# Kernel optimization log

Measured on AMD Instinct MI355X. Metric: run time of the kernel, lower is better.

Reference implementation:

```python
import jax, jax.numpy as jnp
import numpy as np

N = 20000   # nodes
E = 400000  # edges per hop
IN_C = 256
HID = 128
HEADS = 2
OUT_C = 256
RELU_SLOPE = 0.2  # GATConv LeakyReLU negative slope
EPS = 1e-16


def _segment_mean(vals, idx, num_segments):
    s = jax.ops.segment_sum(vals, idx, num_segments=num_segments)
    cnt = jax.ops.segment_sum(jnp.ones((vals.shape[0], 1), vals.dtype), idx,
                              num_segments=num_segments)
    return s / (cnt + EPS)


def _gat(x, src, dst, Wg, a_src, a_dst, bg):
    # x: [N, IN_C] -> h: [N, HEADS, HID]
    h = (x @ Wg).reshape(N, HEADS, HID)
    alpha_s = jnp.sum(h * a_src, axis=-1)  # [N, HEADS]
    alpha_d = jnp.sum(h * a_dst, axis=-1)  # [N, HEADS]
    logits = jax.nn.leaky_relu(alpha_s[src] + alpha_d[dst], RELU_SLOPE)  # [E, HEADS]
    # softmax over incoming edges per destination node
    m = jax.ops.segment_max(logits, dst, num_segments=N)  # [N, HEADS]
    m = jnp.where(jnp.isfinite(m), m, 0.0)
    ex = jnp.exp(logits - m[dst])
    denom = jax.ops.segment_sum(ex, dst, num_segments=N)  # [N, HEADS]
    alpha = ex / (denom[dst] + EPS)  # [E, HEADS]
    msg = h[src] * alpha[..., None]  # [E, HEADS, HID]
    out = jax.ops.segment_sum(msg, dst, num_segments=N)  # [N, HEADS, HID]
    return out.reshape(N, HEADS * HID) + bg


def setup_inputs() -> dict:
    key = jax.random.key(0)
    ks = jax.random.split(key, 16)

    def xav(k, shape):
        fan_in, fan_out = shape[0], shape[-1]
        lim = np.sqrt(6.0 / (fan_in + fan_out)).astype(np.float32)
        return jax.random.uniform(k, shape, jnp.float32, -lim, lim)

    inp = {
        "x": jax.random.normal(ks[0], (N, IN_C), jnp.float32),
        "edge_index_1hop": jax.random.randint(ks[1], (2, E), 0, N),
        "edge_time_1hop": jax.random.uniform(ks[2], (E,), jnp.float32),
        "edge_index_2hop": jax.random.randint(ks[3], (2, E), 0, N),
        "edge_time_2hop": jax.random.uniform(ks[4], (E,), jnp.float32),
        "rel_embeddings": jax.random.normal(ks[5], (N, HID), jnp.float32),
        # GATConv params
        "Wg": xav(ks[6], (IN_C, HEADS * HID)),
        "a_src": jax.random.normal(ks[7], (HEADS, HID), jnp.float32) * 0.1,
        "a_dst": jax.random.normal(ks[8], (HEADS, HID), jnp.float32) * 0.1,
        "bg": jnp.zeros((HEADS * HID,), jnp.float32),
        # linear_transform
        "W_lin": xav(ks[9], (HEADS * HID, OUT_C)),
        "b_lin": jnp.zeros((OUT_C,), jnp.float32),
        # time_gate: in = 2*(OUT_C+1)
        "W_tg": xav(ks[10], (2 * (OUT_C + 1), 1)),
        "b_tg": jnp.zeros((1,), jnp.float32),
        # semantic_gate: in = (OUT_C+1) + HID + 1
        "W_sg": xav(ks[11], (OUT_C + 1 + HID + 1, 1)),
        "b_sg": jnp.zeros((1,), jnp.float32),
    }
    return inp


def reference(x, edge_index_1hop, edge_time_1hop, edge_index_2hop,
              edge_time_2hop, rel_embeddings, Wg, a_src, a_dst, bg,
              W_lin, b_lin, W_tg, b_tg, W_sg, b_sg):
    src1, dst1 = edge_index_1hop[0], edge_index_1hop[1]
    src2, dst2 = edge_index_2hop[0], edge_index_2hop[1]

    # ---- 1-hop aggregation ----
    x_1hop = _gat(x, src1, dst1, Wg, a_src, a_dst, bg) @ W_lin + b_lin  # [N, OUT_C]
    time_e1 = edge_time_1hop[:, None]  # [E, 1]
    node_time = _segment_mean(time_e1, dst1, N)  # [N, 1]
    x_1hop_t = jnp.concatenate([x_1hop, node_time], axis=-1)  # [N, OUT_C+1]

    # ---- semantic gate (per 1-hop edge -> per node) ----
    combined = jnp.concatenate(
        [x_1hop_t[src1], rel_embeddings[dst1], time_e1], axis=-1)  # [E, OUT_C+1+HID+1]
    sem_w_edge = jax.nn.sigmoid(combined @ W_sg + b_sg)  # [E, 1]
    sem_w_node = _segment_mean(sem_w_edge, dst1, N)  # [N, 1]

    # ---- 2-hop aggregation, semantically weighted ----
    x_2hop = _gat(x, src2, dst2, Wg, a_src, a_dst, bg) @ W_lin + b_lin  # [N, OUT_C]
    x_2hop = x_2hop * sem_w_node
    x_2hop_t = jnp.concatenate([x_2hop, node_time], axis=-1)  # [N, OUT_C+1]

    # ---- time-gated fusion ----
    gate_in = jnp.concatenate([x_1hop_t, x_2hop_t], axis=-1)  # [N, 2*(OUT_C+1)]
    g = jax.nn.sigmoid(gate_in @ W_tg + b_tg)  # [N, 1]
    return g * x_2hop_t + (1.0 - g) * x_1hop_t
```

## Files before the change

### kernel.cpp

```cpp
#include <hip/hip_runtime.h>
#include <math.h>

constexpr float EPSF = 1e-16f;
#define MAXDEG 64
#define BINCH 4096
#define NBUCK 64

typedef __attribute__((ext_vector_type(8))) short bfrag;
typedef __attribute__((ext_vector_type(4))) float ffrag;
typedef __attribute__((ext_vector_type(8))) unsigned short ushortv8;

__device__ __forceinline__ float leaky(float v){ return v >= 0.f ? v : 0.2f*v; }

__device__ __forceinline__ ushort f2bf(float f){
  union { float f; unsigned u; } v; v.f = f;
  unsigned r = (v.u + 0x7FFFu + ((v.u >> 16) & 1u)) >> 16;
  return (ushort)r;
}
__device__ __forceinline__ float bf2f(ushort u){
  union { unsigned u; float f; } v; v.u = ((unsigned)u) << 16;
  return v.f;
}

__device__ __forceinline__ float wred_max(float v){
  #pragma unroll
  for (int d = 32; d; d >>= 1) v = fmaxf(v, __shfl_xor(v, d));
  return v;
}
__device__ __forceinline__ float wred_sum(float v){
  #pragma unroll
  for (int d = 32; d; d >>= 1) v += __shfl_xor(v, d);
  return v;
}


__global__ __launch_bounds__(256) void k_prep(const float* __restrict__ Wg, const float* __restrict__ Wlin,
    const float* __restrict__ rel, const float* __restrict__ Wsg,
    ushort* __restrict__ Wgt, ushort* __restrict__ Wlt, float* __restrict__ p2, int N){
  __shared__ float tile[32][33];
  int b = blockIdx.x, t = threadIdx.x;
  if (b < 128){
    const float* W = (b < 64) ? Wg : Wlin;
    ushort* Wt = (b < 64) ? Wgt : Wlt;
    int bb = b & 63;
    int bx = (bb & 7)*32, by = (bb >> 3)*32;
    int tx = t & 31, ty = t >> 5;
    for (int r = ty; r < 32; r += 8) tile[r][tx] = W[(size_t)(by+r)*256 + bx+tx];
    __syncthreads();
    for (int r = ty; r < 32; r += 8) Wt[(size_t)(bx+r)*256 + by+tx] = f2bf(tile[tx][r]);
  } else {
    int node = (b-128)*4 + (t>>6);
    if (node >= N) return;
    int lane = t & 63;
    const float* rr = rel + (size_t)node*128;
    float q = rr[lane]*Wsg[257+lane] + rr[64+lane]*Wsg[321+lane];
    q = wred_sum(q);
    if (lane == 0) p2[node] = q;
  }
}


__global__ __launch_bounds__(256) void k_work1(const float* __restrict__ x, const ushort* __restrict__ Wgt,
    const float* __restrict__ a_src, const float* __restrict__ a_dst,
    ushort* __restrict__ hb, float* __restrict__ as_, float* __restrict__ ad_,
    const int* __restrict__ ei1, const float* __restrict__ et1, const int* __restrict__ ei2,
    int* __restrict__ gcur, int2* __restrict__ bkt1, int2* __restrict__ bkt2,
    int cap1, int cap2, int N, int E1, int E2, int GB1, int B1, int NB){
  __shared__ int hist[NBUCK];
  __shared__ int loff[NBUCK+1];
  __shared__ int cur[NBUCK];
  __shared__ int gbase_s[NBUCK];
  __shared__ int2 stage[BINCH];
  int bid = blockIdx.x, t = threadIdx.x;
  if (bid >= GB1){
    int hop = (bid >= GB1 + B1);
    int cb  = hop ? (bid - GB1 - B1) : (bid - GB1);
    const int* src_arr = hop ? ei2 : ei1;
    const int* dst_arr = hop ? (ei2 + E2) : (ei1 + E1);
    int Eh = hop ? E2 : E1;
    int c0 = cb * BINCH;
    int M = Eh - c0; if (M > BINCH) M = BINCH;
    if (t < NBUCK) hist[t] = 0;
    __syncthreads();
    #pragma unroll
    for (int k = 0; k < BINCH/256; k++){
      int i = k*256 + t;
      if (i < M) atomicAdd(&hist[dst_arr[c0 + i] / NB], 1);
    }
    __syncthreads();
    if (t < NBUCK){
      int v = hist[t];
      int xx = v;
      #pragma unroll
      for (int d = 1; d < NBUCK; d <<= 1){
        int y = __shfl_up(xx, d);
        if (t >= d) xx += y;
      }
      loff[t+1] = xx;
      if (t == 0) loff[0] = 0;
      cur[t] = xx - v;
      gbase_s[t] = atomicAdd(&gcur[hop*NBUCK + t], v);
    }
    __syncthreads();
    #pragma unroll
    for (int k = 0; k < BINCH/256; k++){
      int i = k*256 + t;
      if (i < M){
        int s = src_arr[c0 + i];
        int d = dst_arr[c0 + i];
        int b = d / NB;
        int ld = d - b*NB;
        int pos = atomicAdd(&cur[b], 1);
        float tv = hop ? 0.f : et1[c0 + i];
        stage[pos] = make_int2(s | (ld << 15), __float_as_int(tv));
      }
    }
    __syncthreads();
    int2* bkt = hop ? bkt2 : bkt1;
    int cap = hop ? cap2 : cap1;
    for (int s = t; s < M; s += 256){
      int lo = 0, hi = NBUCK;
      while (hi - lo > 1){ int mid = (lo + hi) >> 1; if (loff[mid] <= s) lo = mid; else hi = mid; }
      int gpos = gbase_s[lo] + (s - loff[lo]);
      if (gpos < cap) bkt[(size_t)lo*cap + gpos] = stage[s];
    }
    return;
  }
  int head = bid & 1;
  int bx = bid >> 1;
  int wid = t >> 6, lane = t & 63;
  int wr = wid >> 1, wc = wid & 1;
  int row0 = bx*128 + wr*64;
  int col0 = head*128 + wc*64;
  int l15 = lane & 15, lk = lane >> 4;
  ffrag acc[4][4];
  #pragma unroll
  for (int i = 0; i < 4; i++)
    #pragma unroll
    for (int j = 0; j < 4; j++){ ffrag z; z[0]=0.f; z[1]=0.f; z[2]=0.f; z[3]=0.f; acc[i][j] = z; }
  for (int kk = 0; kk < 256; kk += 32){
    bfrag a[4], b[4];
    #pragma unroll
    for (int i = 0; i < 4; i++){
      int r = row0 + i*16 + l15; if (r > N-1) r = N-1;
      float4 u0 = *(const float4*)(x + (size_t)r*256 + kk + lk*8);
      float4 u1 = *(const float4*)(x + (size_t)r*256 + kk + lk*8 + 4);
      bfrag tv;
      tv[0]=(short)f2bf(u0.x); tv[1]=(short)f2bf(u0.y); tv[2]=(short)f2bf(u0.z); tv[3]=(short)f2bf(u0.w);
      tv[4]=(short)f2bf(u1.x); tv[5]=(short)f2bf(u1.y); tv[6]=(short)f2bf(u1.z); tv[7]=(short)f2bf(u1.w);
      a[i] = tv;
      int c = col0 + i*16 + l15;
      b[i] = *(const bfrag*)(Wgt + (size_t)c*256 + kk + lk*8);
    }
    #pragma unroll
    for (int i = 0; i < 4; i++)
      #pragma unroll
      for (int j = 0; j < 4; j++)
        acc[i][j] = __builtin_amdgcn_mfma_f32_16x16x32_bf16(a[i], b[j], acc[i][j], 0, 0, 0);
  }
  float asv[4], adv[4];
  #pragma unroll
  for (int j = 0; j < 4; j++){
    int cc = wc*64 + j*16 + l15;
    asv[j] = a_src[head*128 + cc];
    adv[j] = a_dst[head*128 + cc];
  }
  #pragma unroll
  for (int i = 0; i < 4; i++){
    float ps[4] = {0.f,0.f,0.f,0.f}, pd[4] = {0.f,0.f,0.f,0.f};
    #pragma unroll
    for (int j = 0; j < 4; j++){
      int c = col0 + j*16 + l15;
      #pragma unroll
      for (int q = 0; q < 4; q++){
        int r = row0 + i*16 + lk*4 + q;
        float v = acc[i][j][q];
        if (r < N) hb[(size_t)r*256 + c] = f2bf(v);
        ps[q] = fmaf(v, asv[j], ps[q]);
        pd[q] = fmaf(v, adv[j], pd[q]);
      }
    }
    #pragma unroll
    for (int q = 0; q < 4; q++){
      #pragma unroll
      for (int d = 1; d < 16; d <<= 1){
        ps[q] += __shfl_xor(ps[q], d);
        pd[q] += __shfl_xor(pd[q], d);
      }
      int r = row0 + i*16 + lk*4 + q;
      if (l15 == 0 && r < N){
        atomicAdd(&as_[r*2 + head], ps[q]);
        atomicAdd(&ad_[r*2 + head], pd[q]);
      }
    }
  }
}


__global__ __launch_bounds__(256) void k_place(const int* __restrict__ gcur,
    const int2* __restrict__ bkt1, const int2* __restrict__ bkt2, int cap1, int cap2,
    int* __restrict__ ssrc1, int* __restrict__ ssrc2, float* __restrict__ stime1,
    int* __restrict__ cntg, float* __restrict__ ntime, float* __restrict__ p1,
    const float* __restrict__ Wsg, int N, int NB){
  __shared__ int   cnt_l[512];
  __shared__ float ts_l[512];
  int b = blockIdx.x & 63, hop = blockIdx.x >> 6;
  int t = threadIdx.x;
  int nbase = b * NB;
  int ncnt = N - nbase; if (ncnt > NB) ncnt = NB; if (ncnt < 0) ncnt = 0;
  for (int i = t; i < NB; i += 256){ cnt_l[i] = 0; ts_l[i] = 0.f; }
  __syncthreads();
  const int2* bkt = hop ? bkt2 : bkt1;
  int cap = hop ? cap2 : cap1;
  int len = gcur[hop*NBUCK + b]; if (len > cap) len = cap;
  int* ssrc = hop ? ssrc2 : ssrc1;
  for (int i = t; i < len; i += 256){
    int2 en = bkt[(size_t)b*cap + i];
    int src = en.x & 0x7FFF;
    int ld  = en.x >> 15;
    int slot = atomicAdd(&cnt_l[ld], 1);
    if (slot < MAXDEG){
      size_t o = (size_t)(nbase + ld)*MAXDEG + slot;
      ssrc[o] = src;
      if (hop == 0) stime1[o] = __int_as_float(en.y);
    }
    if (hop == 0) atomicAdd(&ts_l[ld], __int_as_float(en.y));
  }
  __syncthreads();
  float w256 = Wsg[256];
  for (int ld = t; ld < ncnt; ld += 256){
    int node = nbase + ld;
    int c = cnt_l[ld];
    cntg[hop*N + node] = c;
    if (hop == 0){
      float nt = ts_l[ld] / ((float)c + EPSF);
      ntime[node] = nt;
      p1[node] = nt * w256;
    }
  }
}


__global__ __launch_bounds__(256) void k_node(const int* __restrict__ cntg,
    const int* __restrict__ ssrc1, const int* __restrict__ ssrc2,
    const float* __restrict__ as_, const float* __restrict__ ad_,
    const ushort* __restrict__ h, const float* __restrict__ bg,
    ushort* __restrict__ gatb, int N, int gN4){
  __shared__ int   s_src[4][MAXDEG];
  __shared__ float2 s_w[4][MAXDEG];
  int wid = threadIdx.x >> 6, lane = threadIdx.x & 63;
  int hop = blockIdx.x >= gN4;
  int node = (blockIdx.x - (hop ? gN4 : 0))*4 + wid;
  bool active = node < N;
  const int* ssrc = hop ? ssrc2 : ssrc1;
  int deg = 0; float ad0 = 0.f, ad1 = 0.f;
  if (active){
    int degt = cntg[hop*N + node];
    deg = degt > MAXDEG ? MAXDEG : degt;
    ad0 = ad_[node*2]; ad1 = ad_[node*2+1];
  }
  size_t o0 = (size_t)node * MAXDEG;
  int msrc = 0;
  float l0 = -INFINITY, l1 = -INFINITY;
  if (lane < deg){
    msrc = ssrc[o0 + lane];
    float2 a = ((const float2*)as_)[msrc];
    l0 = leaky(a.x + ad0); l1 = leaky(a.y + ad1);
  }
  float m0 = wred_max(l0), m1 = wred_max(l1);
  float x0 = 0.f, x1 = 0.f;
  if (lane < deg){ x0 = __expf(l0 - m0); x1 = __expf(l1 - m1); }
  float e0 = wred_sum(x0), e1 = wred_sum(x1);
  float rd0 = 1.f/(e0 + EPSF), rd1 = 1.f/(e1 + EPSF);
  s_src[wid][lane] = msrc;
  s_w[wid][lane] = make_float2(x0*rd0, x1*rd1);
  if (!active) return;
  int eh = lane >> 5, cl = lane & 31, ch0 = cl << 3, head = cl >> 4;
  float acc[8] = {0.f,0.f,0.f,0.f,0.f,0.f,0.f,0.f};
  int i = 0;
  for (; i + 4 <= deg; i += 4){
    int eA = i + eh, eB = i + 2 + eh;
    int sA = s_src[wid][eA], sB = s_src[wid][eB];
    float2 wA2 = s_w[wid][eA], wB2 = s_w[wid][eB];
    float wA = head ? wA2.y : wA2.x;
    float wB = head ? wB2.y : wB2.x;
    ushortv8 uA = *(const ushortv8*)(h + (size_t)sA*256 + ch0);
    ushortv8 uB = *(const ushortv8*)(h + (size_t)sB*256 + ch0);
    #pragma unroll
    for (int k = 0; k < 8; k++) acc[k] = fmaf(wA, bf2f(uA[k]), acc[k]);
    #pragma unroll
    for (int k = 0; k < 8; k++) acc[k] = fmaf(wB, bf2f(uB[k]), acc[k]);
  }
  for (; i < deg; i += 2){
    int e = i + eh;
    bool v = e < deg;
    int s = v ? s_src[wid][e] : 0;
    float w = 0.f;
    if (v){ float2 w2 = s_w[wid][e]; w = head ? w2.y : w2.x; }
    ushortv8 u = *(const ushortv8*)(h + (size_t)s*256 + ch0);
    #pragma unroll
    for (int k = 0; k < 8; k++) acc[k] = fmaf(w, bf2f(u[k]), acc[k]);
  }
  #pragma unroll
  for (int k = 0; k < 8; k++) acc[k] += __shfl_xor(acc[k], 32);
  if (eh == 0){
    float4 b0 = *(const float4*)(bg + ch0);
    float4 b1 = *(const float4*)(bg + ch0 + 4);
    ushortv8 o;
    o[0] = f2bf(acc[0] + b0.x); o[1] = f2bf(acc[1] + b0.y);
    o[2] = f2bf(acc[2] + b0.z); o[3] = f2bf(acc[3] + b0.w);
    o[4] = f2bf(acc[4] + b1.x); o[5] = f2bf(acc[5] + b1.y);
    o[6] = f2bf(acc[6] + b1.z); o[7] = f2bf(acc[7] + b1.w);
    *(ushortv8*)(gatb + (size_t)(hop ? N + node : node)*256 + ch0) = o;
  }
}


__global__ __launch_bounds__(256) void k_gemm2(const ushort* __restrict__ A, const ushort* __restrict__ Bt,
    const float* __restrict__ bias, const float* __restrict__ Wsg,
    float* __restrict__ Cf, float* __restrict__ p1, int M, int N){
  int wid = threadIdx.x >> 6, lane = threadIdx.x & 63;
  int wr = wid >> 1, wc = wid & 1;
  int row0 = blockIdx.x*128 + wr*64;
  int col0 = blockIdx.y*128 + wc*64;
  int l15 = lane & 15, lk = lane >> 4;
  ffrag acc[4][4];
  #pragma unroll
  for (int i = 0; i < 4; i++)
    #pragma unroll
    for (int j = 0; j < 4; j++){ ffrag z; z[0]=0.f; z[1]=0.f; z[2]=0.f; z[3]=0.f; acc[i][j] = z; }
  for (int kk = 0; kk < 256; kk += 32){
    bfrag a[4], b[4];
    #pragma unroll
    for (int i = 0; i < 4; i++){
      int r = row0 + i*16 + l15; if (r > M-1) r = M-1;
      a[i] = *(const bfrag*)(A + (size_t)r*256 + kk + lk*8);
      int c = col0 + i*16 + l15;
      b[i] = *(const bfrag*)(Bt + (size_t)c*256 + kk + lk*8);
    }
    #pragma unroll
    for (int i = 0; i < 4; i++)
      #pragma unroll
      for (int j = 0; j < 4; j++)
        acc[i][j] = __builtin_amdgcn_mfma_f32_16x16x32_bf16(a[i], b[j], acc[i][j], 0, 0, 0);
  }
  float wsv[4]; float bv[4];
  #pragma unroll
  for (int j = 0; j < 4; j++){
    int c = col0 + j*16 + l15;
    wsv[j] = Wsg[c];
    bv[j] = bias[c];
  }
  #pragma unroll
  for (int i = 0; i < 4; i++){
    float ps[4] = {0.f,0.f,0.f,0.f};
    #pragma unroll
    for (int j = 0; j < 4; j++){
      int c = col0 + j*16 + l15;
      #pragma unroll
      for (int q = 0; q < 4; q++){
        int r = row0 + i*16 + lk*4 + q;
        float v = acc[i][j][q] + bv[j];
        if (r < M) Cf[(size_t)r*256 + c] = v;
        ps[q] = fmaf(v, wsv[j], ps[q]);
      }
    }
    #pragma unroll
    for (int q = 0; q < 4; q++){
      #pragma unroll
      for (int d = 1; d < 16; d <<= 1) ps[q] += __shfl_xor(ps[q], d);
      int r = row0 + i*16 + lk*4 + q;
      if (l15 == 0 && r < N) atomicAdd(&p1[r], ps[q]);
    }
  }
}


__global__ __launch_bounds__(256) void k_final(const float* __restrict__ x1, const float* __restrict__ x2r,
    const int* __restrict__ cntg, const int* __restrict__ ssrc1, const float* __restrict__ stime1,
    const float* __restrict__ p1, const float* __restrict__ p2,
    const float* __restrict__ Wsg, const float* __restrict__ bsg,
    const float* __restrict__ ntime, const float* __restrict__ Wtg, const float* __restrict__ btg,
    float* __restrict__ out, int N){
  int node = blockIdx.x*4 + (threadIdx.x>>6);
  if (node >= N) return;
  int lane = threadIdx.x & 63;
  int degt = cntg[node];
  int deg = degt > MAXDEG ? MAXDEG : degt;
  float acc = 0.f;
  if (lane < deg){
    size_t o = (size_t)node*MAXDEG + lane;
    float z = p1[ssrc1[o]] + p2[node] + bsg[0] + stime1[o]*Wsg[385];
    acc = 1.f / (1.f + __expf(-z));
  }
  acc = wred_sum(acc);
  float sm = acc / ((float)degt + EPSF);
  float nt = ntime[node];
  int c0 = lane << 2;
  float4 a4 = *(const float4*)(x1  + (size_t)node*256 + c0);
  float4 r4 = *(const float4*)(x2r + (size_t)node*256 + c0);
  float4 b4; b4.x = r4.x*sm; b4.y = r4.y*sm; b4.z = r4.z*sm; b4.w = r4.w*sm;
  float4 w1 = *(const float4*)(Wtg + c0);
  float4 w2 = *(const float4*)(Wtg + 257 + c0);
  float s = a4.x*w1.x + a4.y*w1.y + a4.z*w1.z + a4.w*w1.w
          + b4.x*w2.x + b4.y*w2.y + b4.z*w2.z + b4.w*w2.w;
  if (lane == 0) s += nt*Wtg[256] + nt*Wtg[513] + btg[0];
  s = wred_sum(s);
  float g = 1.f / (1.f + __expf(-s));
  float* orow = out + (size_t)node*257;
  orow[c0+0] = g*b4.x + (1.f - g)*a4.x;
  orow[c0+1] = g*b4.y + (1.f - g)*a4.y;
  orow[c0+2] = g*b4.z + (1.f - g)*a4.z;
  orow[c0+3] = g*b4.w + (1.f - g)*a4.w;
  if (lane == 0) orow[256] = nt;
}


extern "C" void kernel_launch(void* const* d_in, const int* in_sizes, int n_in,
                              void* d_out, int out_size, void* d_ws, size_t ws_size,
                              hipStream_t stream){
  const float* x    = (const float*)d_in[0];
  const int*   ei1  = (const int*)d_in[1];
  const float* et1  = (const float*)d_in[2];
  const int*   ei2  = (const int*)d_in[3];
  const float* rel  = (const float*)d_in[5];
  const float* Wg   = (const float*)d_in[6];
  const float* asrc = (const float*)d_in[7];
  const float* adst = (const float*)d_in[8];
  const float* bg   = (const float*)d_in[9];
  const float* Wlin = (const float*)d_in[10];
  const float* blin = (const float*)d_in[11];
  const float* Wtg  = (const float*)d_in[12];
  const float* btg  = (const float*)d_in[13];
  const float* Wsg  = (const float*)d_in[14];
  const float* bsg  = (const float*)d_in[15];
  float* out = (float*)d_out;

  const int N  = in_sizes[0] / 256;
  const int E1 = in_sizes[1] / 2;
  const int E2 = in_sizes[3] / 2;
  const int NB = (N + NBUCK - 1) / NBUCK;
  const int cap1 = E1/NBUCK + 2048;
  const int cap2 = E2/NBUCK + 2048;

  char* base = (char*)d_ws;
  size_t off = 0;
  auto alloc = [&](size_t bytes)->char*{
    char* p = base + off;
    off += (bytes + 255) & ~(size_t)255;
    return p;
  };
  int*    gcur  = (int*)alloc((size_t)2*NBUCK*4);
  float*  as_   = (float*)alloc((size_t)2*N*4);
  float*  ad_   = (float*)alloc((size_t)2*N*4);
  size_t zero_bytes = off;
  ushort* Wgt   = (ushort*)alloc((size_t)256*256*2);
  ushort* Wlt   = (ushort*)alloc((size_t)256*256*2);
  ushort* hb    = (ushort*)alloc((size_t)N*256*2);
  ushort* gatb  = (ushort*)alloc((size_t)2*N*256*2);
  float*  x12   = (float*)alloc((size_t)2*N*256*4);
  float*  ntime = (float*)alloc((size_t)N*4);
  float*  p1    = (float*)alloc((size_t)N*4);
  float*  p2    = (float*)alloc((size_t)N*4);
  int*    cntg  = (int*)alloc((size_t)2*N*4);
  int*    ssrc1 = (int*)alloc((size_t)N*MAXDEG*4);
  int*    ssrc2 = (int*)alloc((size_t)N*MAXDEG*4);
  float*  stime1= (float*)alloc((size_t)N*MAXDEG*4);
  int2*   bkt1  = (int2*)alloc((size_t)NBUCK*cap1*8);
  int2*   bkt2  = (int2*)alloc((size_t)NBUCK*cap2*8);

  dim3 blk(256);
  int gN4 = (N + 3) / 4;
  int GB1 = ((N + 127) / 128) * 2;
  int B1  = (E1 + BINCH - 1) / BINCH;
  int B2  = (E2 + BINCH - 1) / BINCH;
  dim3 ggemm2((2*N + 127) / 128, 2);

  hipMemsetAsync(d_ws, 0, zero_bytes, stream);
  k_prep<<<128 + gN4, blk, 0, stream>>>(Wg, Wlin, rel, Wsg, Wgt, Wlt, p2, N);
  k_work1<<<GB1 + B1 + B2, blk, 0, stream>>>(x, Wgt, asrc, adst, hb, as_, ad_,
                                             ei1, et1, ei2, gcur, bkt1, bkt2,
                                             cap1, cap2, N, E1, E2, GB1, B1, NB);
  k_place<<<128, blk, 0, stream>>>(gcur, bkt1, bkt2, cap1, cap2, ssrc1, ssrc2, stime1,
                                   cntg, ntime, p1, Wsg, N, NB);
  k_node<<<2*gN4, blk, 0, stream>>>(cntg, ssrc1, ssrc2, as_, ad_, hb, bg, gatb, N, gN4);
  k_gemm2<<<ggemm2, blk, 0, stream>>>(gatb, Wlt, blin, Wsg, x12, p1, 2*N, N);
  k_final<<<gN4, blk, 0, stream>>>(x12, x12 + (size_t)N*256, cntg, ssrc1, stime1,
                                   p1, p2, Wsg, bsg, ntime, Wtg, btg, out, N);
}
```

Before: 158.1 us.

## Store GEMM2 output in bf16, fold workspace zeroing into prep, unroll gather

The second GEMM now writes its output to an intermediate buffer as bf16 instead of fp32, and the final kernel reads bf16 and converts, halving that buffer's traffic. The hipMemsetAsync is replaced by extra blocks in k_prep that zero the workspace, removing a separate memset launch. The node aggregation loop gains an 8-edge unrolled body that issues four gathers per lane at once to raise memory-level parallelism. The cost is reduced precision of the intermediate x1/x2 values and higher register pressure.

After: 149.4 us. -5.5%, faster.

```diff
diff --git a/kernel.cpp b/kernel.cpp
--- a/kernel.cpp
+++ b/kernel.cpp
@@ -36,20 +36,25 @@
 
 __global__ __launch_bounds__(256) void k_prep(const float* __restrict__ Wg, const float* __restrict__ Wlin,
     const float* __restrict__ rel, const float* __restrict__ Wsg,
-    ushort* __restrict__ Wgt, ushort* __restrict__ Wlt, float* __restrict__ p2, int N){
+    ushort* __restrict__ Wgt, ushort* __restrict__ Wlt, float* __restrict__ p2,
+    float4* __restrict__ zbase, int znum4, int ZB, int N){
   __shared__ float tile[32][33];
   int b = blockIdx.x, t = threadIdx.x;
-  if (b < 128){
-    const float* W = (b < 64) ? Wg : Wlin;
-    ushort* Wt = (b < 64) ? Wgt : Wlt;
-    int bb = b & 63;
+  if (b < ZB){
+    int idx = b*256 + t;
+    if (idx < znum4) zbase[idx] = make_float4(0.f,0.f,0.f,0.f);
+  } else if (b < ZB + 128){
+    int bb = b - ZB;
+    const float* W = (bb < 64) ? Wg : Wlin;
+    ushort* Wt = (bb < 64) ? Wgt : Wlt;
+    bb &= 63;
     int bx = (bb & 7)*32, by = (bb >> 3)*32;
     int tx = t & 31, ty = t >> 5;
     for (int r = ty; r < 32; r += 8) tile[r][tx] = W[(size_t)(by+r)*256 + bx+tx];
     __syncthreads();
     for (int r = ty; r < 32; r += 8) Wt[(size_t)(bx+r)*256 + by+tx] = f2bf(tile[tx][r]);
   } else {
-    int node = (b-128)*4 + (t>>6);
+    int node = (b-ZB-128)*4 + (t>>6);
     if (node >= N) return;
     int lane = t & 63;
     const float* rr = rel + (size_t)node*128;
@@ -278,6 +283,29 @@
   int eh = lane >> 5, cl = lane & 31, ch0 = cl << 3, head = cl >> 4;
   float acc[8] = {0.f,0.f,0.f,0.f,0.f,0.f,0.f,0.f};
   int i = 0;
+  for (; i + 8 <= deg; i += 8){
+    int eA = i + eh, eB = i + 2 + eh, eC = i + 4 + eh, eD = i + 6 + eh;
+    int sA = s_src[wid][eA], sB = s_src[wid][eB];
+    int sC = s_src[wid][eC], sD = s_src[wid][eD];
+    float2 wA2 = s_w[wid][eA], wB2 = s_w[wid][eB];
+    float2 wC2 = s_w[wid][eC], wD2 = s_w[wid][eD];
+    float wA = head ? wA2.y : wA2.x;
+    float wB = head ? wB2.y : wB2.x;
+    float wC = head ? wC2.y : wC2.x;
+    float wD = head ? wD2.y : wD2.x;
+    ushortv8 uA = *(const ushortv8*)(h + (size_t)sA*256 + ch0);
+    ushortv8 uB = *(const ushortv8*)(h + (size_t)sB*256 + ch0);
+    ushortv8 uC = *(const ushortv8*)(h + (size_t)sC*256 + ch0);
+    ushortv8 uD = *(const ushortv8*)(h + (size_t)sD*256 + ch0);
+    #pragma unroll
+    for (int k = 0; k < 8; k++) acc[k] = fmaf(wA, bf2f(uA[k]), acc[k]);
+    #pragma unroll
+    for (int k = 0; k < 8; k++) acc[k] = fmaf(wB, bf2f(uB[k]), acc[k]);
+    #pragma unroll
+    for (int k = 0; k < 8; k++) acc[k] = fmaf(wC, bf2f(uC[k]), acc[k]);
+    #pragma unroll
+    for (int k = 0; k < 8; k++) acc[k] = fmaf(wD, bf2f(uD[k]), acc[k]);
+  }
   for (; i + 4 <= deg; i += 4){
     int eA = i + eh, eB = i + 2 + eh;
     int sA = s_src[wid][eA], sB = s_src[wid][eB];
@@ -318,7 +346,7 @@
 
 __global__ __launch_bounds__(256) void k_gemm2(const ushort* __restrict__ A, const ushort* __restrict__ Bt,
     const float* __restrict__ bias, const float* __restrict__ Wsg,
-    float* __restrict__ Cf, float* __restrict__ p1, int M, int N){
+    ushort* __restrict__ Cb, float* __restrict__ p1, int M, int N){
   int wid = threadIdx.x >> 6, lane = threadIdx.x & 63;
   int wr = wid >> 1, wc = wid & 1;
   int row0 = blockIdx.x*128 + wr*64;
@@ -361,7 +389,7 @@
       for (int q = 0; q < 4; q++){
         int r = row0 + i*16 + lk*4 + q;
         float v = acc[i][j][q] + bv[j];
-        if (r < M) Cf[(size_t)r*256 + c] = v;
+        if (r < M) Cb[(size_t)r*256 + c] = f2bf(v);
         ps[q] = fmaf(v, wsv[j], ps[q]);
       }
     }
@@ -376,7 +404,7 @@
 }
 
 
-__global__ __launch_bounds__(256) void k_final(const float* __restrict__ x1, const float* __restrict__ x2r,
+__global__ __launch_bounds__(256) void k_final(const ushort* __restrict__ x1, const ushort* __restrict__ x2r,
     const int* __restrict__ cntg, const int* __restrict__ ssrc1, const float* __restrict__ stime1,
     const float* __restrict__ p1, const float* __restrict__ p2,
     const float* __restrict__ Wsg, const float* __restrict__ bsg,
@@ -397,9 +425,10 @@
   float sm = acc / ((float)degt + EPSF);
   float nt = ntime[node];
   int c0 = lane << 2;
-  float4 a4 = *(const float4*)(x1  + (size_t)node*256 + c0);
-  float4 r4 = *(const float4*)(x2r + (size_t)node*256 + c0);
-  float4 b4; b4.x = r4.x*sm; b4.y = r4.y*sm; b4.z = r4.z*sm; b4.w = r4.w*sm;
+  ushort4 au = *(const ushort4*)(x1  + (size_t)node*256 + c0);
+  ushort4 ru = *(const ushort4*)(x2r + (size_t)node*256 + c0);
+  float4 a4 = make_float4(bf2f(au.x), bf2f(au.y), bf2f(au.z), bf2f(au.w));
+  float4 b4; b4.x = bf2f(ru.x)*sm; b4.y = bf2f(ru.y)*sm; b4.z = bf2f(ru.z)*sm; b4.w = bf2f(ru.w)*sm;
   float4 w1 = *(const float4*)(Wtg + c0);
   float4 w2 = *(const float4*)(Wtg + 257 + c0);
   float s = a4.x*w1.x + a4.y*w1.y + a4.z*w1.z + a4.w*w1.w
@@ -458,7 +487,7 @@
   ushort* Wlt   = (ushort*)alloc((size_t)256*256*2);
   ushort* hb    = (ushort*)alloc((size_t)N*256*2);
   ushort* gatb  = (ushort*)alloc((size_t)2*N*256*2);
-  float*  x12   = (float*)alloc((size_t)2*N*256*4);
+  ushort* x12   = (ushort*)alloc((size_t)2*N*256*2);
   float*  ntime = (float*)alloc((size_t)N*4);
   float*  p1    = (float*)alloc((size_t)N*4);
   float*  p2    = (float*)alloc((size_t)N*4);
@@ -474,10 +503,12 @@
   int GB1 = ((N + 127) / 128) * 2;
   int B1  = (E1 + BINCH - 1) / BINCH;
   int B2  = (E2 + BINCH - 1) / BINCH;
+  int znum4 = (int)(zero_bytes / 16);
+  int ZB = (znum4 + 255) / 256;
   dim3 ggemm2((2*N + 127) / 128, 2);
 
-  hipMemsetAsync(d_ws, 0, zero_bytes, stream);
-  k_prep<<<128 + gN4, blk, 0, stream>>>(Wg, Wlin, rel, Wsg, Wgt, Wlt, p2, N);
+  k_prep<<<ZB + 128 + gN4, blk, 0, stream>>>(Wg, Wlin, rel, Wsg, Wgt, Wlt, p2,
+                                             (float4*)d_ws, znum4, ZB, N);
   k_work1<<<GB1 + B1 + B2, blk, 0, stream>>>(x, Wgt, asrc, adst, hb, as_, ad_,
                                              ei1, et1, ei2, gcur, bkt1, bkt2,
                                              cap1, cap2, N, E1, E2, GB1, B1, NB);
```
